# Kernel optimization log

Hardware: AMD Instinct MI355X
Metric: run time of the kernel (lower is better)

The kernel has to match this reference:

```python
import jax, jax.numpy as jnp
import numpy as np

K = 3
TAPS = K * K
STD = float(np.sqrt(2.0)) / K  # FilterNorm scale: relu gain / kernel_size


def filter_norm(f, axis):
    # torch FilterNorm: subtract mean, divide by unbiased std (+1e-10), scale by STD
    m = jnp.mean(f, axis=axis, keepdims=True)
    sd = jnp.std(f, axis=axis, keepdims=True, ddof=1)
    return (f - m) / (sd + 1e-10) * STD


def setup_inputs() -> dict:
    key = jax.random.key(0)
    ks = jax.random.split(key, 9)
    B, C, H, W = 4, 64, 192, 192
    mid = int(C * 0.2)  # se_ratio=0.2 -> 12
    f = lambda k, shape, s: jax.random.normal(k, shape, jnp.float32) * s
    return {
        'x':   f(ks[0], (B, C, H, W), 1.0),
        'sw':  f(ks[1], (TAPS, C), 0.05),        # spatial branch 1x1 conv weight
        'sb':  f(ks[2], (TAPS,), 0.05),
        'cw1': f(ks[3], (mid, C), 0.05),         # channel branch squeeze
        'cb1': f(ks[4], (mid,), 0.05),
        'cw2': f(ks[5], (C * TAPS, mid), 0.05),  # channel branch expand
        'cb2': f(ks[6], (C * TAPS,), 0.05),
        'w2':  f(ks[7], (C, C, 1, 9), 0.05),     # trailing 1x9 conv
        'b2':  f(ks[8], (C,), 0.05),
    }


def block_forward(x, sw, sb, cw1, cb1, cw2, cb2, w2, b2):
    B, C, H, W = x.shape
    # --- DDFPack ---
    # spatial filters: 1x1 conv -> (B, 9, H, W), FilterNorm across the 9 taps
    s = jnp.einsum('bchw,tc->bthw', x, sw) + sb[None, :, None, None]
    s = filter_norm(s, axis=1)
    # channel filters: GAP -> 1x1 -> relu -> 1x1 -> (B, C, 9), FilterNorm over taps
    g = x.mean(axis=(2, 3))                         # (B, C)
    h1 = jax.nn.relu(g @ cw1.T + cb1)               # (B, mid)
    cf = (h1 @ cw2.T + cb2).reshape(B, C, TAPS)     # (B, C, 9)
    cf = filter_norm(cf, axis=2)
    # decoupled dynamic filter apply: per-pixel depthwise 3x3, combine='mul', pad=1
    xp = jnp.pad(x, ((0, 0), (0, 0), (1, 1), (1, 1)))
    out = jnp.zeros_like(x)
    for idx in range(TAPS):  # fixed 9-tap loop, no big unfold intermediate
        i, j = idx // K, idx % K
        out = out + xp[:, :, i:i + H, j:j + W] * s[:, idx:idx + 1] * cf[:, :, idx, None, None]
    # --- LeakyReLU(0.1) -> 1x9 conv (pad (0,4)) -> residual add (res_scale=1) ---
    a = jnp.where(out >= 0, out, 0.1 * out)
    y = jax.lax.conv_general_dilated(a, w2, (1, 1), ((0, 0), (4, 4)),
                                     dimension_numbers=('NCHW', 'OIHW', 'NCHW'))
    y = y + b2[None, :, None, None]
    return x + y


def reference(x, sw, sb, cw1, cb1, cw2, cb2, w2, b2):
    return block_forward(x, sw, sb, cw1, cb1, cw2, cb2, w2, b2)
```

## Files before the change

### kernel.cpp

```cpp
#include <hip/hip_runtime.h>
#include <hip/hip_bf16.h>

#define B_    4
#define C_    64
#define H_    192
#define W_    192
#define TAPS_ 9
#define MID_  12
#define HW_   (H_ * W_)
#define K_TOT 576
#define AT_STRIDE 72

constexpr float STD_ = 0.47140452079103173f;

using bf16 = __hip_bfloat16;
typedef __attribute__((ext_vector_type(4))) float  f32x4;
typedef __attribute__((ext_vector_type(8))) short  short8;

__device__ __forceinline__ unsigned short f2bf_bits(float v) {
    union { bf16 h; unsigned short u; } cv;
    cv.h = __float2bfloat16(v);
    return cv.u;
}

__device__ __forceinline__ int at_word(int row, int cw) {
    int key = (row >> 2) & 7;
    return row * (AT_STRIDE / 2) + ((((cw >> 2) ^ key) & 7) << 2) + (cw & 3);
}

__global__ __launch_bounds__(256) void k_pre(const float* __restrict__ x,
                                             const float* __restrict__ w2,
                                             unsigned short* __restrict__ w2bf,
                                             float* __restrict__ partials) {
    int bx = blockIdx.x;
    if (bx < 144) {
        int d = bx * 256 + threadIdx.x;
        int o = d / K_TOT;
        int rem = d - o * K_TOT;
        int t = rem >> 6;
        int c = rem & 63;
        w2bf[d] = f2bf_bits(w2[(o * C_ + c) * TAPS_ + t]);
        return;
    }
    bx -= 144;
    int bc = bx / 3, part = bx - 3 * (bx / 3);
    const float4* p = (const float4*)(x + (size_t)bc * HW_ + part * 12288);
    float s = 0.f;
    #pragma unroll
    for (int k = 0; k < 12; ++k) {
        float4 u = p[threadIdx.x + k * 256];
        s += u.x + u.y + u.z + u.w;
    }
    #pragma unroll
    for (int off = 32; off; off >>= 1) s += __shfl_down(s, off);
    __shared__ float red[4];
    if ((threadIdx.x & 63) == 0) red[threadIdx.x >> 6] = s;
    __syncthreads();
    if (threadIdx.x == 0)
        partials[bx] = red[0] + red[1] + red[2] + red[3];
}

__global__ __launch_bounds__(256, 3) void k_main(const float* __restrict__ x,
                                                 const float* __restrict__ sw,
                                                 const float* __restrict__ sb,
                                                 const float* __restrict__ partials,
                                                 const float* __restrict__ cw1,
                                                 const float* __restrict__ cb1,
                                                 const float* __restrict__ cw2,
                                                 const float* __restrict__ cb2,
                                                 const unsigned short* __restrict__ w2bf,
                                                 const float* __restrict__ bias2,
                                                 float* __restrict__ out) {
    __shared__ __align__(16) char smem[38624];
    short*          aT    = (short*)smem;
    unsigned*       aT32  = (unsigned*)smem;
    float*          sw_l  = (float*)smem;
    float*          s_l   = (float*)(smem + 28800);
    float*          b2_l  = (float*)(smem + 35712);
    float*          sb_l  = (float*)(smem + 35968);
    float*          cfn_l = (float*)(smem + 36016);
    float*          h1_l  = (float*)(smem + 38320);
    float*          g_l   = (float*)(smem + 38368);

    int bx = blockIdx.x;
    int bh = (bx & 7) * 96 + (bx >> 3);
    int bb = bh / H_;
    int h  = bh - bb * H_;
    int tid = threadIdx.x;
    int lane = tid & 63, wid = tid >> 6;
    int quad = lane >> 4, l16 = lane & 15;
    int obase = wid * 16;
    int w0 = 4 * lane;

    for (int i = tid; i < TAPS_ * C_; i += 256) sw_l[i] = sw[i];
    if (tid < C_) b2_l[tid] = bias2[tid];
    if (tid < TAPS_) sb_l[tid] = sb[tid];
    __syncthreads();

    const short* w2s = (const short*)w2bf;
    const short* arow = w2s + (obase + l16) * K_TOT + quad * 8;
    short8 a0 = *(const short8*)(arow);
    short8 a1 = *(const short8*)(arow + 32);

    long ro0 = (long)((h > 0) ? (h - 1) : h) * W_;
    long ro1 = (long)h * W_;
    long ro2 = (long)((h < H_ - 1) ? (h + 1) : h) * W_;
    const float* xc = x + (size_t)bb * C_ * HW_;

    float4 P0a, P1a, P2a, P0b, P1b, P2b;
    if (lane < 48) {
        const float* q0 = xc + (size_t)(wid * 16) * HW_;
        const float* q1 = q0 + HW_;
        P0a = *(const float4*)(q0 + ro0 + w0);
        P1a = *(const float4*)(q0 + ro1 + w0);
        P2a = *(const float4*)(q0 + ro2 + w0);
        P0b = *(const float4*)(q1 + ro0 + w0);
        P1b = *(const float4*)(q1 + ro1 + w0);
        P2b = *(const float4*)(q1 + ro2 + w0);
    }

    if (tid < W_) {
        int w = tid;
        float acc[TAPS_];
        #pragma unroll
        for (int t = 0; t < TAPS_; ++t) acc[t] = sb_l[t];
        const float* px = x + (size_t)bb * C_ * HW_ + h * W_ + w;
        float xv0[8], xv1[8];
        #pragma unroll
        for (int j = 0; j < 8; ++j) xv0[j] = px[(size_t)j * HW_];
        #pragma unroll
        for (int j = 0; j < 8; ++j) xv1[j] = px[(size_t)(8 + j) * HW_];
        __builtin_amdgcn_sched_barrier(0);

#define FMA8(XV, CB)                                                           \
        do {                                                                   \
            _Pragma("unroll")                                                  \
            for (int j = 0; j < 8; ++j)                                        \
                _Pragma("unroll")                                              \
                for (int t = 0; t < TAPS_; ++t)                                \
                    acc[t] = fmaf(XV[j], sw_l[t * C_ + (CB) + j], acc[t]);     \
        } while (0)
#define LOAD8(XV, CB)                                                          \
        do {                                                                   \
            _Pragma("unroll")                                                  \
            for (int j = 0; j < 8; ++j) XV[j] = px[(size_t)((CB) + j) * HW_];  \
        } while (0)

        FMA8(xv0, 0);   LOAD8(xv0, 16); __builtin_amdgcn_sched_barrier(0);
        FMA8(xv1, 8);   LOAD8(xv1, 24); __builtin_amdgcn_sched_barrier(0);
        FMA8(xv0, 16);  LOAD8(xv0, 32); __builtin_amdgcn_sched_barrier(0);
        FMA8(xv1, 24);  LOAD8(xv1, 40); __builtin_amdgcn_sched_barrier(0);
        FMA8(xv0, 32);  LOAD8(xv0, 48); __builtin_amdgcn_sched_barrier(0);
        FMA8(xv1, 40);  LOAD8(xv1, 56); __builtin_amdgcn_sched_barrier(0);
        FMA8(xv0, 48);
        FMA8(xv1, 56);
#undef FMA8
#undef LOAD8

        float mean = 0.f;
        #pragma unroll
        for (int t = 0; t < TAPS_; ++t) mean += acc[t];
        mean *= (1.f / TAPS_);
        float var = 0.f;
        #pragma unroll
        for (int t = 0; t < TAPS_; ++t) { float d = acc[t] - mean; var += d * d; }
        var *= (1.f / (TAPS_ - 1));
        float scale = STD_ / (sqrtf(fmaxf(var, 0.f)) + 1e-10f);
        float* sp = s_l + (w & 3) * 432 + (w >> 2);
        #pragma unroll
        for (int t = 0; t < TAPS_; ++t) sp[t * 48] = (acc[t] - mean) * scale;
    } else {
        int c = lane;
        const float* pp = partials + (bb * C_ + c) * 3;
        g_l[c] = (pp[0] + pp[1] + pp[2]) * (1.0f / HW_);
        if (c < MID_) {
            float acc = cb1[c];
            #pragma unroll 8
            for (int cc = 0; cc < C_; ++cc) acc += g_l[cc] * cw1[c * C_ + cc];
            h1_l[c] = fmaxf(acc, 0.f);
        }
        float f[TAPS_];
        float mean = 0.f;
        #pragma unroll
        for (int t = 0; t < TAPS_; ++t) {
            int n = c * TAPS_ + t;
            float acc = cb2[n];
            #pragma unroll
            for (int m = 0; m < MID_; ++m) acc += h1_l[m] * cw2[n * MID_ + m];
            f[t] = acc;
            mean += acc;
        }
        mean *= (1.f / TAPS_);
        float var = 0.f;
        #pragma unroll
        for (int t = 0; t < TAPS_; ++t) { float d = f[t] - mean; var += d * d; }
        var *= (1.f / (TAPS_ - 1));
        float scale = STD_ / (sqrtf(fmaxf(var, 0.f)) + 1e-10f);
        #pragma unroll
        for (int t = 0; t < TAPS_; ++t)
            cfn_l[c * TAPS_ + t] = (f[t] - mean) * scale;
    }
    __syncthreads();

    for (int i = tid; i < 8 * (AT_STRIDE / 2); i += 256) {
        int rowIdx = i / (AT_STRIDE / 2);
        int col    = i - rowIdx * (AT_STRIDE / 2);
        int r = (rowIdx < 4) ? rowIdx : (192 + rowIdx);
        aT32[r * (AT_STRIDE / 2) + col] = 0u;
    }

    {
        if (lane < 48) {
            float sreg[4][TAPS_];
            #pragma unroll
            for (int k = 0; k < 4; ++k) {
                const float* sp = s_l + k * 432 + lane;
                #pragma unroll
                for (int t = 0; t < TAPS_; ++t) sreg[k][t] = sp[t * 48];
            }
            bool l0 = (lane == 0), l47 = (lane == 47);
            float rok0f = (h > 0)      ? 1.f : 0.f;
            float rok2f = (h < H_ - 1) ? 1.f : 0.f;

#define TAPROW(RR, FA, FB)                                                     \
            do {                                                               \
                float ma = __shfl_up(FA.w, 1);   ma = l0  ? 0.f : ma;          \
                float mb = __shfl_up(FB.w, 1);   mb = l0  ? 0.f : mb;          \
                float pa = __shfl_down(FA.x, 1); pa = l47 ? 0.f : pa;          \
                float pb = __shfl_down(FB.x, 1); pb = l47 ? 0.f : pb;          \
                float va[6] = { ma, FA.x, FA.y, FA.z, FA.w, pa };              \
                float vb[6] = { mb, FB.x, FB.y, FB.z, FB.w, pb };              \
                _Pragma("unroll")                                              \
                for (int dc = 0; dc < 3; ++dc) {                               \
                    int t = (RR) * 3 + dc;                                     \
                    float cva = cfp[t];                                        \
                    float cvb = cfp[TAPS_ + t];                                \
                    _Pragma("unroll")                                          \
                    for (int k = 0; k < 4; ++k) {                              \
                        acc0[k] = fmaf(va[k + dc] * sreg[k][t], cva, acc0[k]); \
                        acc1[k] = fmaf(vb[k + dc] * sreg[k][t], cvb, acc1[k]); \
                    }                                                          \
                }                                                              \
            } while (0)

            #pragma unroll 1
            for (int i = 0; i < 16; i += 2) {
                int c0 = wid * 16 + i;
                int cu = __builtin_amdgcn_readfirstlane(c0);
                const float* cfp = cfn_l + cu * TAPS_;
                float4 C0a = P0a, C1a = P1a, C2a = P2a;
                float4 C0b = P0b, C1b = P1b, C2b = P2b;
                if (i < 14) {
                    const float* q0 = xc + (size_t)(c0 + 2) * HW_;
                    const float* q1 = q0 + HW_;
                    P0a = *(const float4*)(q0 + ro0 + w0);
                    P1a = *(const float4*)(q0 + ro1 + w0);
                    P2a = *(const float4*)(q0 + ro2 + w0);
                    P0b = *(const float4*)(q1 + ro0 + w0);
                    P1b = *(const float4*)(q1 + ro1 + w0);
                    P2b = *(const float4*)(q1 + ro2 + w0);
                }
                __builtin_amdgcn_sched_barrier(0);
                C0a.x *= rok0f; C0a.y *= rok0f; C0a.z *= rok0f; C0a.w *= rok0f;
                C0b.x *= rok0f; C0b.y *= rok0f; C0b.z *= rok0f; C0b.w *= rok0f;
                C2a.x *= rok2f; C2a.y *= rok2f; C2a.z *= rok2f; C2a.w *= rok2f;
                C2b.x *= rok2f; C2b.y *= rok2f; C2b.z *= rok2f; C2b.w *= rok2f;
                float acc0[4] = {0.f, 0.f, 0.f, 0.f};
                float acc1[4] = {0.f, 0.f, 0.f, 0.f};
                TAPROW(0, C0a, C0b);
                TAPROW(1, C1a, C1b);
                TAPROW(2, C2a, C2b);
                int cw = c0 >> 1;
                #pragma unroll
                for (int k = 0; k < 4; ++k) {
                    float a0v = acc0[k]; a0v = (a0v >= 0.f) ? a0v : 0.1f * a0v;
                    float a1v = acc1[k]; a1v = (a1v >= 0.f) ? a1v : 0.1f * a1v;
                    unsigned pk = (unsigned)f2bf_bits(a0v)
                                | ((unsigned)f2bf_bits(a1v) << 16);
                    aT32[at_word(w0 + k + 4, cw)] = pk;
                }
            }
#undef TAPROW
        }
    }
    __syncthreads();

    {
        f32x4 acc[12];
        #pragma unroll
        for (int n = 0; n < 12; ++n) acc[n] = (f32x4){0.f, 0.f, 0.f, 0.f};

        #pragma unroll 1
        for (int kk = 0; kk < 18; ++kk) {
            short8 a2 = a1;
            if (kk < 16) a2 = *(const short8*)(arow + (kk + 2) * 32);
            int t = kk >> 1;
            int ch = ((kk & 1) << 2) + quad;
            int rowb = l16 + t;
            int key0 = (rowb >> 2) & 7;
            int off0 = rowb * AT_STRIDE + (((ch ^ key0) & 7) << 3);
            int off1 = rowb * AT_STRIDE + (((ch ^ key0 ^ 4) & 7) << 3);
            #pragma unroll
            for (int n = 0; n < 12; ++n) {
                int off = ((n & 1) ? off1 : off0) + n * 16 * AT_STRIDE;
                short8 bf = *(const short8*)(aT + off);
                acc[n] = __builtin_amdgcn_mfma_f32_16x16x32_bf16(a0, bf, acc[n], 0, 0, 0);
            }
            a0 = a1; a1 = a2;
        }

        size_t xbase = (size_t)bb * C_ * HW_ + (size_t)h * W_;
        #pragma unroll
        for (int n = 0; n < 12; ++n) {
            int w = n * 16 + l16;
            #pragma unroll
            for (int reg = 0; reg < 4; ++reg) {
                int o = obase + quad * 4 + reg;
                size_t idx = xbase + (size_t)o * HW_ + w;
                out[idx] = acc[n][reg] + b2_l[o] + x[idx];
            }
        }
    }
}

extern "C" void kernel_launch(void* const* d_in, const int* in_sizes, int n_in,
                              void* d_out, int out_size, void* d_ws, size_t ws_size,
                              hipStream_t stream) {
    const float* x   = (const float*)d_in[0];
    const float* sw  = (const float*)d_in[1];
    const float* sb  = (const float*)d_in[2];
    const float* cw1 = (const float*)d_in[3];
    const float* cb1 = (const float*)d_in[4];
    const float* cw2 = (const float*)d_in[5];
    const float* cb2 = (const float*)d_in[6];
    const float* w2  = (const float*)d_in[7];
    const float* b2  = (const float*)d_in[8];
    float* out = (float*)d_out;

    unsigned short* w2bf = (unsigned short*)d_ws;
    float* partials = (float*)((char*)d_ws + 73728);

    hipLaunchKernelGGL(k_pre, dim3(912), dim3(256), 0, stream, x, w2, w2bf, partials);
    hipLaunchKernelGGL(k_main, dim3(B_ * H_), dim3(256), 0, stream,
                       x, sw, sb, partials, cw1, cb1, cw2, cb2, w2bf, b2, out);
}
```

Measured before the change: 139.4 us.

## Retile 1x9 conv MFMA so each wave covers two output-channel groups

```diff
diff --git a/kernel.cpp b/kernel.cpp
--- a/kernel.cpp
+++ b/kernel.cpp
@@ -89,18 +89,12 @@
     int tid = threadIdx.x;
     int lane = tid & 63, wid = tid >> 6;
     int quad = lane >> 4, l16 = lane & 15;
-    int obase = wid * 16;
     int w0 = 4 * lane;
 
     for (int i = tid; i < TAPS_ * C_; i += 256) sw_l[i] = sw[i];
     if (tid < C_) b2_l[tid] = bias2[tid];
     if (tid < TAPS_) sb_l[tid] = sb[tid];
     __syncthreads();
-
-    const short* w2s = (const short*)w2bf;
-    const short* arow = w2s + (obase + l16) * K_TOT + quad * 8;
-    short8 a0 = *(const short8*)(arow);
-    short8 a1 = *(const short8*)(arow + 32);
 
     long ro0 = (long)((h > 0) ? (h - 1) : h) * W_;
     long ro1 = (long)h * W_;
@@ -286,38 +280,62 @@
     __syncthreads();
 
     {
-        f32x4 acc[12];
-        #pragma unroll
-        for (int n = 0; n < 12; ++n) acc[n] = (f32x4){0.f, 0.f, 0.f, 0.f};
+        size_t xbase = (size_t)bb * C_ * HW_ + (size_t)h * W_;
+        int oh = (wid & 1) * 32;
+        int wq = wid >> 1;
+        const short* arow0 = (const short*)w2bf + (oh      + l16) * K_TOT + quad * 8;
+        const short* arow1 = (const short*)w2bf + (oh + 16 + l16) * K_TOT + quad * 8;
 
         #pragma unroll 1
-        for (int kk = 0; kk < 18; ++kk) {
-            short8 a2 = a1;
-            if (kk < 16) a2 = *(const short8*)(arow + (kk + 2) * 32);
-            int t = kk >> 1;
-            int ch = ((kk & 1) << 2) + quad;
-            int rowb = l16 + t;
-            int key0 = (rowb >> 2) & 7;
-            int off0 = rowb * AT_STRIDE + (((ch ^ key0) & 7) << 3);
-            int off1 = rowb * AT_STRIDE + (((ch ^ key0 ^ 4) & 7) << 3);
+        for (int half = 0; half < 2; ++half) {
+            int ntile0 = half * 6 + wq * 3;
+            f32x4 acc[2][3];
             #pragma unroll
-            for (int n = 0; n < 12; ++n) {
-                int off = ((n & 1) ? off1 : off0) + n * 16 * AT_STRIDE;
-                short8 bf = *(const short8*)(aT + off);
-                acc[n] = __builtin_amdgcn_mfma_f32_16x16x32_bf16(a0, bf, acc[n], 0, 0, 0);
+            for (int g = 0; g < 2; ++g)
+                #pragma unroll
+                for (int j = 0; j < 3; ++j) acc[g][j] = (f32x4){0.f, 0.f, 0.f, 0.f};
+            short8 a0g0 = *(const short8*)(arow0);
+            short8 a1g0 = *(const short8*)(arow0 + 32);
+            short8 a0g1 = *(const short8*)(arow1);
+            short8 a1g1 = *(const short8*)(arow1 + 32);
+
+            #pragma unroll 1
+            for (int kk = 0; kk < 18; ++kk) {
+                short8 a2g0 = a1g0, a2g1 = a1g1;
+                if (kk < 16) {
+                    a2g0 = *(const short8*)(arow0 + (kk + 2) * 32);
+                    a2g1 = *(const short8*)(arow1 + (kk + 2) * 32);
+                }
+                int t = kk >> 1;
+                int ch = ((kk & 1) << 2) + quad;
+                int rowb = l16 + t;
+                int key0 = (rowb >> 2) & 7;
+                int off0 = rowb * AT_STRIDE + (((ch ^ key0) & 7) << 3);
+                int off1 = rowb * AT_STRIDE + (((ch ^ key0 ^ 4) & 7) << 3);
+                #pragma unroll
+                for (int j = 0; j < 3; ++j) {
+                    int n = ntile0 + j;
+                    int off = ((n & 1) ? off1 : off0) + n * 16 * AT_STRIDE;
+                    short8 bf = *(const short8*)(aT + off);
+                    acc[0][j] = __builtin_amdgcn_mfma_f32_16x16x32_bf16(a0g0, bf, acc[0][j], 0, 0, 0);
+                    acc[1][j] = __builtin_amdgcn_mfma_f32_16x16x32_bf16(a0g1, bf, acc[1][j], 0, 0, 0);
+                }
+                a0g0 = a1g0; a1g0 = a2g0;
+                a0g1 = a1g1; a1g1 = a2g1;
             }
-            a0 = a1; a1 = a2;
-        }
-
-        size_t xbase = (size_t)bb * C_ * HW_ + (size_t)h * W_;
-        #pragma unroll
-        for (int n = 0; n < 12; ++n) {
-            int w = n * 16 + l16;
+
             #pragma unroll
-            for (int reg = 0; reg < 4; ++reg) {
-                int o = obase + quad * 4 + reg;
-                size_t idx = xbase + (size_t)o * HW_ + w;
-                out[idx] = acc[n][reg] + b2_l[o] + x[idx];
+            for (int g = 0; g < 2; ++g) {
+                #pragma unroll
+                for (int j = 0; j < 3; ++j) {
+                    int w = (ntile0 + j) * 16 + l16;
+                    #pragma unroll
+                    for (int reg = 0; reg < 4; ++reg) {
+                        int o = oh + g * 16 + quad * 4 + reg;
+                        size_t idx = xbase + (size_t)o * HW_ + w;
+                        out[idx] = acc[g][j][reg] + b2_l[o] + x[idx];
+                    }
+                }
             }
         }
     }
```

Measured after the change: 142.1 us. No clear change (+2.0%).
